# Optimization experiments

Measured on AMD Instinct MI355X. Metric: run time of the kernel, lower is better.

The kernel has to match this reference:

```python
import jax, jax.numpy as jnp
import numpy as np

EPS = 1e-5
H = 6  # num_heads

def batchnorm(x, g, b):
    # BatchNorm1d over node dim using batch statistics (biased var, eps=1e-5)
    mu = x.mean(0)
    var = jnp.mean((x - mu) ** 2, 0)
    return (x - mu) * jax.lax.rsqrt(var + EPS) * g + b

def setup_inputs() -> dict:
    key = jax.random.key(0)
    ks = jax.random.split(key, 16)
    N, E, D = 20000, 200000, 384
    DH = 2 * D  # mlp hidden = dim * mlp_ratio(2.0)
    s = 0.05
    lin = lambda k, i, o: jax.random.normal(k, (i, o), jnp.float32) * s
    inp = {}
    inp['x'] = jax.random.normal(ks[0], (N, D), jnp.float32)
    inp['edge_index'] = jax.random.randint(ks[1], (2, E), 0, N)
    inp['edge_attr'] = jax.random.normal(ks[2], (E, D), jnp.float32)
    # norm1
    inp['g1'] = jnp.ones((D,), jnp.float32); inp['b1'] = jnp.zeros((D,), jnp.float32)
    # TransformerConv-style attention (concat=True, beta=False, edge_dim=D)
    inp['Wq'] = lin(ks[3], D, D); inp['bq'] = jnp.zeros((D,), jnp.float32)
    inp['Wk'] = lin(ks[4], D, D); inp['bk'] = jnp.zeros((D,), jnp.float32)
    inp['Wv'] = lin(ks[5], D, D); inp['bv'] = jnp.zeros((D,), jnp.float32)
    inp['We'] = lin(ks[6], D, D)  # lin_edge, no bias
    inp['Wskip'] = lin(ks[7], D, D); inp['bskip'] = jnp.zeros((D,), jnp.float32)
    # norm2
    inp['g2'] = jnp.ones((D,), jnp.float32); inp['b2'] = jnp.zeros((D,), jnp.float32)
    # Mlp
    inp['W1'] = lin(ks[8], D, DH); inp['bm1'] = jnp.zeros((DH,), jnp.float32)
    inp['W2'] = lin(ks[9], DH, D); inp['bm2'] = jnp.zeros((D,), jnp.float32)
    return inp

def reference(x, edge_index, edge_attr, g1, b1, Wq, bq, Wk, bk, Wv, bv, We, Wskip, bskip, g2, b2, W1, bm1, W2, bm2):
    N, D = x.shape
    Dh = D // H
    scale = 1.0 / jnp.sqrt(jnp.float32(Dh))
    h = batchnorm(x, g1, b1)
    q = (h @ Wq + bq).reshape(N, H, Dh)
    k = (h @ Wk + bk).reshape(N, H, Dh)
    v = (h @ Wv + bv).reshape(N, H, Dh)
    e = (edge_attr @ We).reshape(-1, H, Dh)  # [E,H,Dh]
    src, dst = edge_index[0], edge_index[1]
    ke = k[src] + e  # edge attr added to key
    ve = v[src] + e  # and to value (PyG TransformerConv)
    logits = jnp.einsum('ehd,ehd->eh', q[dst], ke) * scale  # [E,H]
    # segment softmax over incoming edges of each dst node
    m = jax.ops.segment_max(logits, dst, num_segments=N)
    a = jnp.exp(logits - m[dst])
    ssum = jax.ops.segment_sum(a, dst, num_segments=N)
    denom = ssum[dst]
    a = a / jnp.where(denom == 0, 1.0, denom)
    agg = jax.ops.segment_sum(a[:, :, None] * ve, dst, num_segments=N).reshape(N, D)
    attn = agg + (h @ Wskip + bskip)  # root skip (lin_skip)
    x = x + attn  # residual 1 (drop_path/dropout disabled in eval)
    h2 = batchnorm(x, g2, b2)
    mlp = jax.nn.gelu(h2 @ W1 + bm1, approximate=False) @ W2 + bm2
    return x + mlp
```

## Files before the change

kernel.cpp:

```cpp
#include <hip/hip_runtime.h>
#include <hip/hip_bf16.h>

#define DD 384
#define NH 6
#define DHID 768

typedef __attribute__((ext_vector_type(8))) short bf16x8;
typedef __attribute__((ext_vector_type(4))) float f32x4;

__device__ __forceinline__ void gload_lds16(const void* gsrc, void* ldst) {
  __builtin_amdgcn_global_load_lds((const __attribute__((address_space(1))) void*)gsrc,
                                   (__attribute__((address_space(3))) void*)ldst,
                                   16, 0, 0);
}

__device__ __forceinline__ float b2f(unsigned short u) {
  union { unsigned int i; float f; } c;
  c.i = (unsigned int)u << 16;
  return c.f;
}

__device__ __forceinline__ short f2bf(float x) {
  union { __hip_bfloat16 h; short s; } u;
  u.h = __float2bfloat16(x);
  return u.s;
}

__global__ __launch_bounds__(384) void bn_stats_k(const float* __restrict__ x, float* __restrict__ sums,
                                                  float* __restrict__ sq, int N, int rpb) {
  int d = threadIdx.x;
  int r0 = blockIdx.x * rpb;
  int r1 = min(r0 + rpb, N);
  float s = 0.f, ss = 0.f;
  for (int r = r0; r < r1; ++r) {
    float v = x[(size_t)r * DD + d];
    s += v; ss += v * v;
  }
  atomicAdd(&sums[d], s);
  atomicAdd(&sq[d], ss);
}

__global__ void bn_finalize_k(const float* sums, const float* sq, const float* g, const float* b,
                              float* a, float* c, int N) {
  int d = blockIdx.x * blockDim.x + threadIdx.x;
  if (d >= DD) return;
  float inv = 1.f / (float)N;
  float mu = sums[d] * inv;
  float var = sq[d] * inv - mu * mu;
  float rs = rsqrtf(var + 1e-5f);
  a[d] = rs * g[d];
  c[d] = b[d] - mu * rs * g[d];
}

union BPack { ushort4 u; __hip_bfloat16 b[4]; };

__global__ void norm_to_bf16_k(const float* __restrict__ x, const float* __restrict__ a,
                               const float* __restrict__ c, __hip_bfloat16* __restrict__ h, int total4) {
  int i = blockIdx.x * blockDim.x + threadIdx.x;
  if (i >= total4) return;
  float4 v = ((const float4*)x)[i];
  int d0 = (i * 4) % DD;
  float4 av = *(const float4*)(a + d0);
  float4 cv = *(const float4*)(c + d0);
  BPack p;
  p.b[0] = __float2bfloat16(v.x * av.x + cv.x);
  p.b[1] = __float2bfloat16(v.y * av.y + cv.y);
  p.b[2] = __float2bfloat16(v.z * av.z + cv.z);
  p.b[3] = __float2bfloat16(v.w * av.w + cv.w);
  ((ushort4*)h)[i] = p.u;
}

__global__ void transpose_bf16_k(const float* __restrict__ in, __hip_bfloat16* __restrict__ out,
                                 int K, int Nout) {
  int i = blockIdx.x * blockDim.x + threadIdx.x;
  if (i >= K * Nout) return;
  int k = i / Nout, n = i % Nout;
  out[(size_t)n * K + k] = __float2bfloat16(in[i]);
}

__global__ void concat_bias_k(const float* bq, const float* bk, const float* bv, const float* bs,
                              float* out) {
  int i = blockIdx.x * blockDim.x + threadIdx.x;
  if (i >= 1536) return;
  float v = (i < 384) ? bq[i] : (i < 768) ? bk[i - 384] : (i < 1152) ? bv[i - 768] : bs[i - 1152];
  out[i] = v;
}

__global__ void add3_k(const float* __restrict__ x, const float* __restrict__ agg,
                       const float* __restrict__ skip, float* __restrict__ x1, int total4) {
  int i = blockIdx.x * blockDim.x + threadIdx.x;
  if (i >= total4) return;
  float4 a = ((const float4*)x)[i];
  float4 b = ((const float4*)agg)[i];
  float4 c = ((const float4*)skip)[i];
  float4 o;
  o.x = a.x + b.x + c.x; o.y = a.y + b.y + c.y;
  o.z = a.z + b.z + c.z; o.w = a.w + b.w + c.w;
  ((float4*)x1)[i] = o;
}

__global__ void hist_k(const int* __restrict__ ei, int* __restrict__ deg, int E) {
  int i = blockIdx.x * blockDim.x + threadIdx.x;
  if (i < E) atomicAdd(&deg[ei[E + i]], 1);
}

__global__ __launch_bounds__(1024) void scan_k(const int* __restrict__ deg, int* __restrict__ row_start,
                                               int* __restrict__ cursor, int N) {
  __shared__ int part[1024];
  int t = threadIdx.x;
  int ch = (N + 1023) / 1024;
  int c0 = t * ch, c1 = min(c0 + ch, N);
  int s = 0;
  for (int i = c0; i < c1; ++i) s += deg[i];
  part[t] = s;
  __syncthreads();
  for (int off = 1; off < 1024; off <<= 1) {
    int v = (t >= off) ? part[t - off] : 0;
    __syncthreads();
    part[t] += v;
    __syncthreads();
  }
  int run = part[t] - s;
  for (int i = c0; i < c1; ++i) {
    row_start[i] = run; cursor[i] = run; run += deg[i];
  }
  if (t == 1023) row_start[N] = part[1023];
}

__global__ void scatter_k(const int* __restrict__ ei, int* __restrict__ cursor,
                          int* __restrict__ csr_src, int* __restrict__ csr_eid, int E) {
  int i = blockIdx.x * blockDim.x + threadIdx.x;
  if (i >= E) return;
  int s = ei[i], d = ei[E + i];
  int pos = atomicAdd(&cursor[d], 1);
  csr_src[pos] = s;
  csr_eid[pos] = i;
}

__global__ __launch_bounds__(256) void attn_k(const __hip_bfloat16* __restrict__ qkv,
                                              const __hip_bfloat16* __restrict__ ebuf,
                                              const int* __restrict__ row_start,
                                              const int* __restrict__ csr_src,
                                              const int* __restrict__ csr_eid,
                                              float* __restrict__ agg, int N) {
  int wid = (blockIdx.x * blockDim.x + threadIdx.x) >> 6;
  int lane = threadIdx.x & 63;
  if (wid >= N) return;
  int g = lane >> 4, l = lane & 15;
  const ushort* qk = (const ushort*)qkv;
  const ushort* eu = (const ushort*)ebuf;
  float q[NH][4], acc[NH][4], psum[NH];
#pragma unroll
  for (int h = 0; h < NH; ++h) {
    ushort4 u = *(const ushort4*)&qk[(size_t)wid * 1152 + h * 64 + l * 4];
    q[h][0] = b2f(u.x); q[h][1] = b2f(u.y); q[h][2] = b2f(u.z); q[h][3] = b2f(u.w);
#pragma unroll
    for (int j = 0; j < 4; ++j) acc[h][j] = 0.f;
    psum[h] = 0.f;
  }
  int i0 = row_start[wid], i1 = row_start[wid + 1];
  for (int i = i0; i < i1; i += 4) {
    int e = i + g;
    bool valid = e < i1;
    int ec = valid ? e : i1 - 1;
    size_t sb = (size_t)csr_src[ec] * 1152;
    size_t eb = (size_t)csr_eid[ec] * 384;
    float ev[NH][4], p[NH];
#pragma unroll
    for (int h = 0; h < NH; ++h) {
      ushort4 ue = *(const ushort4*)&eu[eb + h * 64 + l * 4];
      ev[h][0] = b2f(ue.x); ev[h][1] = b2f(ue.y); ev[h][2] = b2f(ue.z); ev[h][3] = b2f(ue.w);
      ushort4 uk = *(const ushort4*)&qk[sb + 384 + h * 64 + l * 4];
      float t = q[h][0] * (b2f(uk.x) + ev[h][0]);
      t += q[h][1] * (b2f(uk.y) + ev[h][1]);
      t += q[h][2] * (b2f(uk.z) + ev[h][2]);
      t += q[h][3] * (b2f(uk.w) + ev[h][3]);
      t += __shfl_xor(t, 1);
      t += __shfl_xor(t, 2);
      t += __shfl_xor(t, 4);
      t += __shfl_xor(t, 8);
      p[h] = valid ? __expf(t * 0.125f) : 0.f;
    }
#pragma unroll
    for (int h = 0; h < NH; ++h) {
      ushort4 uv = *(const ushort4*)&qk[sb + 768 + h * 64 + l * 4];
      acc[h][0] += p[h] * (b2f(uv.x) + ev[h][0]);
      acc[h][1] += p[h] * (b2f(uv.y) + ev[h][1]);
      acc[h][2] += p[h] * (b2f(uv.z) + ev[h][2]);
      acc[h][3] += p[h] * (b2f(uv.w) + ev[h][3]);
      psum[h] += p[h];
    }
  }
#pragma unroll
  for (int h = 0; h < NH; ++h) {
#pragma unroll
    for (int j = 0; j < 4; ++j) {
      acc[h][j] += __shfl_xor(acc[h][j], 16);
      acc[h][j] += __shfl_xor(acc[h][j], 32);
    }
    psum[h] += __shfl_xor(psum[h], 16);
    psum[h] += __shfl_xor(psum[h], 32);
  }
  if (lane < 16) {
#pragma unroll
    for (int h = 0; h < NH; ++h) {
      float inv = psum[h] > 0.f ? 1.f / psum[h] : 0.f;
      float4 o;
      o.x = acc[h][0] * inv; o.y = acc[h][1] * inv;
      o.z = acc[h][2] * inv; o.w = acc[h][3] * inv;
      *(float4*)&agg[(size_t)wid * DD + h * 64 + l * 4] = o;
    }
  }
}

#define BM 128
#define BN 128
#define BK 64

enum { M_QKVS = 0, M_BF16 = 1, M_GELU = 2, M_RES = 3 };

template <int MODE>
__global__ __launch_bounds__(256) void gemm_k(const __hip_bfloat16* __restrict__ A,
                                              const __hip_bfloat16* __restrict__ BT,
                                              const float* __restrict__ bias,
                                              const float* __restrict__ res,
                                              void* __restrict__ out0, void* __restrict__ out1,
                                              int M, int K, int Nn) {
  __shared__ short lA[BM * BK];
  __shared__ short lB[BN * BK];
  int t = threadIdx.x;
  int lane = t & 63, w = t >> 6;
  int wr = (w >> 1) * 64, wc = (w & 1) * 64;
  int row0 = blockIdx.y * BM, col0 = blockIdx.x * BN;
  int lr = lane & 15, lk = lane >> 4;
  f32x4 acc[4][4] = {};

  for (int kt = 0; kt < K; kt += BK) {
    __syncthreads();
#pragma unroll
    for (int j = 0; j < 4; ++j) {
      int c = j * 256 + t;
      int r = c >> 3;
      int kcs = (c & 7) ^ (r & 7);
      int wavebase = (j * 256 + w * 64) * 8;
      int gra = row0 + r; gra = gra < M ? gra : M - 1;
      gload_lds16(A + (size_t)gra * K + kt + kcs * 8, &lA[wavebase]);
      gload_lds16(BT + (size_t)(col0 + r) * K + kt + kcs * 8, &lB[wavebase]);
    }
    __syncthreads();
#pragma unroll
    for (int kk = 0; kk < 2; ++kk) {
      int p = (kk * 4 + lk) ^ (lr & 7);
      bf16x8 af[4], bfr[4];
#pragma unroll
      for (int mi = 0; mi < 4; ++mi)
        af[mi] = *(const bf16x8*)&lA[(wr + mi * 16 + lr) * BK + p * 8];
#pragma unroll
      for (int ni = 0; ni < 4; ++ni)
        bfr[ni] = *(const bf16x8*)&lB[(wc + ni * 16 + lr) * BK + p * 8];
#pragma unroll
      for (int mi = 0; mi < 4; ++mi)
#pragma unroll
        for (int ni = 0; ni < 4; ++ni)
          acc[mi][ni] = __builtin_amdgcn_mfma_f32_16x16x32_bf16(af[mi], bfr[ni], acc[mi][ni], 0, 0, 0);
    }
  }

#pragma unroll
  for (int mi = 0; mi < 4; ++mi) {
#pragma unroll
    for (int r = 0; r < 4; ++r) {
      int row = row0 + wr + mi * 16 + lk * 4 + r;
      if (row >= M) continue;
#pragma unroll
      for (int ni = 0; ni < 4; ++ni) {
        int col = col0 + wc + ni * 16 + lr;
        float v = acc[mi][ni][r];
        if constexpr (MODE == M_QKVS) {
          v += bias[col];
          if (col < 1152)
            ((__hip_bfloat16*)out0)[(size_t)row * 1152 + col] = __float2bfloat16(v);
          else
            ((float*)out1)[(size_t)row * DD + (col - 1152)] = v;
        } else if constexpr (MODE == M_BF16) {
          ((__hip_bfloat16*)out0)[(size_t)row * Nn + col] = __float2bfloat16(v);
        } else if constexpr (MODE == M_GELU) {
          v += bias[col];
          v = 0.5f * v * (1.f + erff(v * 0.70710678118f));
          ((__hip_bfloat16*)out0)[(size_t)row * Nn + col] = __float2bfloat16(v);
        } else {
          v += bias[col];
          ((float*)out0)[(size_t)row * Nn + col] = v + res[(size_t)row * Nn + col];
        }
      }
    }
  }
}

__global__ __launch_bounds__(256, 2) void gemm_edge_wide(const float* __restrict__ A,
                                                         const __hip_bfloat16* __restrict__ BT,
                                                         __hip_bfloat16* __restrict__ out, int M) {
  __shared__ short lA[BM * BK];
  __shared__ short lB[DD * BK];
  int t = threadIdx.x;
  int lane = t & 63, w = t >> 6;
  int wr = (w >> 1) * 64, wc = (w & 1) * 192;
  int row0 = blockIdx.x * BM;
  int lr = lane & 15, lk = lane >> 4;
  f32x4 acc[4][12] = {};

  for (int kt = 0; kt < DD; kt += BK) {
    __syncthreads();
#pragma unroll
    for (int pss = 0; pss < 12; ++pss) {
      int c = pss * 256 + t;
      int r = c >> 3;
      int kcs = (c & 7) ^ (r & 7);
      int wavebase = (pss * 256 + w * 64) * 8;
      gload_lds16(BT + (size_t)r * DD + kt + kcs * 8, &lB[wavebase]);
    }
#pragma unroll
    for (int pss = 0; pss < 4; ++pss) {
      int c = pss * 256 + t;
      int r = c >> 3, kcl = c & 7;
      int gra = row0 + r; gra = gra < M ? gra : M - 1;
      const float4* ap = (const float4*)(A + (size_t)gra * DD + kt + kcl * 8);
      float4 f0 = ap[0], f1 = ap[1];
      bf16x8 v;
      v[0] = f2bf(f0.x); v[1] = f2bf(f0.y); v[2] = f2bf(f0.z); v[3] = f2bf(f0.w);
      v[4] = f2bf(f1.x); v[5] = f2bf(f1.y); v[6] = f2bf(f1.z); v[7] = f2bf(f1.w);
      *(__shared__ bf16x8*)&lA[r * BK + (kcl ^ (r & 7)) * 8] = v;
    }
    __syncthreads();
#pragma unroll
    for (int kk = 0; kk < 2; ++kk) {
      int p = (kk * 4 + lk) ^ (lr & 7);
      bf16x8 af[4];
#pragma unroll
      for (int mi = 0; mi < 4; ++mi)
        af[mi] = *(const bf16x8*)&lA[(wr + mi * 16 + lr) * BK + p * 8];
#pragma unroll
      for (int ni = 0; ni < 12; ++ni) {
        bf16x8 bfr = *(const bf16x8*)&lB[(wc + ni * 16 + lr) * BK + p * 8];
#pragma unroll
        for (int mi = 0; mi < 4; ++mi)
          acc[mi][ni] = __builtin_amdgcn_mfma_f32_16x16x32_bf16(af[mi], bfr, acc[mi][ni], 0, 0, 0);
      }
    }
  }

#pragma unroll
  for (int mi = 0; mi < 4; ++mi) {
#pragma unroll
    for (int r = 0; r < 4; ++r) {
      int row = row0 + wr + mi * 16 + lk * 4 + r;
      if (row >= M) continue;
#pragma unroll
      for (int ni = 0; ni < 12; ++ni) {
        int col = wc + ni * 16 + lr;
        out[(size_t)row * DD + col] = __float2bfloat16(acc[mi][ni][r]);
      }
    }
  }
}

extern "C" void kernel_launch(void* const* d_in, const int* in_sizes, int n_in,
                              void* d_out, int out_size, void* d_ws, size_t ws_size,
                              hipStream_t stream) {
  const float* x   = (const float*)d_in[0];
  const int*   ei  = (const int*)d_in[1];
  const float* ea  = (const float*)d_in[2];
  const float* g1  = (const float*)d_in[3];
  const float* b1  = (const float*)d_in[4];
  const float* Wq  = (const float*)d_in[5];
  const float* bq  = (const float*)d_in[6];
  const float* Wk  = (const float*)d_in[7];
  const float* bk  = (const float*)d_in[8];
  const float* Wv  = (const float*)d_in[9];
  const float* bv  = (const float*)d_in[10];
  const float* We  = (const float*)d_in[11];
  const float* Wsk = (const float*)d_in[12];
  const float* bsk = (const float*)d_in[13];
  const float* g2  = (const float*)d_in[14];
  const float* b2  = (const float*)d_in[15];
  const float* W1  = (const float*)d_in[16];
  const float* bm1 = (const float*)d_in[17];
  const float* W2  = (const float*)d_in[18];
  const float* bm2 = (const float*)d_in[19];

  int N = in_sizes[0] / DD;
  int E = in_sizes[1] / 2;

  char* ws = (char*)d_ws;
  size_t off = 0;
  auto alloc = [&](size_t bytes) -> char* {
    char* p = ws + off;
    off = (off + bytes + 255) & ~(size_t)255;
    return p;
  };

  float* bnsum = (float*)alloc(4 * DD * sizeof(float));
  float* a1 = (float*)alloc(DD * 4);
  float* c1 = (float*)alloc(DD * 4);
  float* a2 = (float*)alloc(DD * 4);
  float* c2 = (float*)alloc(DD * 4);
  float* bqkvs = (float*)alloc(1536 * 4);
  __hip_bfloat16* WqkvsT = (__hip_bfloat16*)alloc((size_t)1536 * DD * 2);
  __hip_bfloat16* WeT = (__hip_bfloat16*)alloc((size_t)DD * DD * 2);
  __hip_bfloat16* W1T = (__hip_bfloat16*)alloc((size_t)DHID * DD * 2);
  __hip_bfloat16* W2T = (__hip_bfloat16*)alloc((size_t)DD * DHID * 2);
  __hip_bfloat16* hbuf = (__hip_bfloat16*)alloc((size_t)N * DD * 2);
  __hip_bfloat16* qkv = (__hip_bfloat16*)alloc((size_t)N * 1152 * 2);
  float* skip = (float*)alloc((size_t)N * DD * 4);
  __hip_bfloat16* ebuf = (__hip_bfloat16*)alloc((size_t)E * DD * 2);
  float* agg = (float*)alloc((size_t)N * DD * 4);
  float* x1 = (float*)alloc((size_t)N * DD * 4);
  __hip_bfloat16* hid = (__hip_bfloat16*)alloc((size_t)N * DHID * 2);
  int* deg = (int*)alloc((size_t)N * 4);
  int* cursor = (int*)alloc((size_t)N * 4);
  int* row_start = (int*)alloc((size_t)(N + 1) * 4);
  int* csr_src = (int*)alloc((size_t)E * 4);
  int* csr_eid = (int*)alloc((size_t)E * 4);
  (void)ws_size; (void)n_in; (void)out_size;

  hipMemsetAsync(bnsum, 0, 4 * DD * sizeof(float), stream);
  hipMemsetAsync(deg, 0, (size_t)N * 4, stream);

  int rpb = 128, sgrid = (N + rpb - 1) / rpb;
  bn_stats_k<<<sgrid, DD, 0, stream>>>(x, bnsum, bnsum + DD, N, rpb);
  bn_finalize_k<<<2, 256, 0, stream>>>(bnsum, bnsum + DD, g1, b1, a1, c1, N);

  int t4 = N * DD / 4;
  norm_to_bf16_k<<<(t4 + 255) / 256, 256, 0, stream>>>(x, a1, c1, hbuf, t4);

  int wgrid = (DD * DD + 255) / 256;
  transpose_bf16_k<<<wgrid, 256, 0, stream>>>(Wq, WqkvsT, DD, DD);
  transpose_bf16_k<<<wgrid, 256, 0, stream>>>(Wk, WqkvsT + (size_t)DD * DD, DD, DD);
  transpose_bf16_k<<<wgrid, 256, 0, stream>>>(Wv, WqkvsT + (size_t)2 * DD * DD, DD, DD);
  transpose_bf16_k<<<wgrid, 256, 0, stream>>>(Wsk, WqkvsT + (size_t)3 * DD * DD, DD, DD);
  transpose_bf16_k<<<wgrid, 256, 0, stream>>>(We, WeT, DD, DD);
  transpose_bf16_k<<<(DD * DHID + 255) / 256, 256, 0, stream>>>(W1, W1T, DD, DHID);
  transpose_bf16_k<<<(DHID * DD + 255) / 256, 256, 0, stream>>>(W2, W2T, DHID, DD);
  concat_bias_k<<<6, 256, 0, stream>>>(bq, bk, bv, bsk, bqkvs);

  dim3 gqkvs(1536 / BN, (N + BM - 1) / BM);
  gemm_k<M_QKVS><<<gqkvs, 256, 0, stream>>>(hbuf, WqkvsT, bqkvs, nullptr, qkv, skip, N, DD, 1536);

  gemm_edge_wide<<<(E + BM - 1) / BM, 256, 0, stream>>>(ea, WeT, ebuf, E);

  hist_k<<<(E + 255) / 256, 256, 0, stream>>>(ei, deg, E);
  scan_k<<<1, 1024, 0, stream>>>(deg, row_start, cursor, N);
  scatter_k<<<(E + 255) / 256, 256, 0, stream>>>(ei, cursor, csr_src, csr_eid, E);

  attn_k<<<(N * 64 + 255) / 256, 256, 0, stream>>>(qkv, ebuf, row_start, csr_src, csr_eid, agg, N);

  add3_k<<<(t4 + 255) / 256, 256, 0, stream>>>(x, agg, skip, x1, t4);

  bn_stats_k<<<sgrid, DD, 0, stream>>>(x1, bnsum + 2 * DD, bnsum + 3 * DD, N, rpb);
  bn_finalize_k<<<2, 256, 0, stream>>>(bnsum + 2 * DD, bnsum + 3 * DD, g2, b2, a2, c2, N);
  norm_to_bf16_k<<<(t4 + 255) / 256, 256, 0, stream>>>(x1, a2, c2, hbuf, t4);

  dim3 gm1(DHID / BN, (N + BM - 1) / BM);
  gemm_k<M_GELU><<<gm1, 256, 0, stream>>>(hbuf, W1T, bm1, nullptr, hid, nullptr, N, DD, DHID);

  dim3 gm2(DD / BN, (N + BM - 1) / BM);
  gemm_k<M_RES><<<gm2, 256, 0, stream>>>(hid, W2T, bm2, x1, (float*)d_out, nullptr, N, DHID, DD);
}
```

Before: 605.5 us.

## Double-buffer LDS in GEMM kernels and load fp32 edge tiles directly to LDS

Both GEMM kernels now use two LDS buffers with BK halved to 32, prefetching the next K-tile with global_load_lds while MFMAs run on the current tile, and use one barrier per iteration. The edge GEMM also stops converting fp32 edge_attr to bf16 in registers before writing to LDS. It now DMA-loads the fp32 tile straight into a swizzled LDS buffer and converts to bf16 when building fragments. The aim is to hide global load latency and the register round-trip, at the cost of twice as many K iterations and barriers. The B tile also loses its XOR swizzle, which may cause LDS bank conflicts.

```diff
diff --git a/kernel.cpp b/kernel.cpp
--- a/kernel.cpp
+++ b/kernel.cpp
@@ -215,7 +215,7 @@
 
 #define BM 128
 #define BN 128
-#define BK 64
+#define BK 32
 
 enum { M_QKVS = 0, M_BF16 = 1, M_GELU = 2, M_RES = 3 };
 
@@ -226,8 +226,8 @@
                                               const float* __restrict__ res,
                                               void* __restrict__ out0, void* __restrict__ out1,
                                               int M, int K, int Nn) {
-  __shared__ short lA[BM * BK];
-  __shared__ short lB[BN * BK];
+  __shared__ short lA[2][BM * BK];
+  __shared__ short lB[2][BN * BK];
   int t = threadIdx.x;
   int lane = t & 63, w = t >> 6;
   int wr = (w >> 1) * 64, wc = (w & 1) * 64;
@@ -235,35 +235,39 @@
   int lr = lane & 15, lk = lane >> 4;
   f32x4 acc[4][4] = {};
 
-  for (int kt = 0; kt < K; kt += BK) {
-    __syncthreads();
-#pragma unroll
-    for (int j = 0; j < 4; ++j) {
-      int c = j * 256 + t;
-      int r = c >> 3;
-      int kcs = (c & 7) ^ (r & 7);
+  auto stage = [&](int b, int kt) {
+#pragma unroll
+    for (int j = 0; j < 2; ++j) {
+      int chunk = j * 256 + t;
+      int r = chunk >> 2, kc = chunk & 3;
       int wavebase = (j * 256 + w * 64) * 8;
       int gra = row0 + r; gra = gra < M ? gra : M - 1;
-      gload_lds16(A + (size_t)gra * K + kt + kcs * 8, &lA[wavebase]);
-      gload_lds16(BT + (size_t)(col0 + r) * K + kt + kcs * 8, &lB[wavebase]);
-    }
-    __syncthreads();
-#pragma unroll
-    for (int kk = 0; kk < 2; ++kk) {
-      int p = (kk * 4 + lk) ^ (lr & 7);
-      bf16x8 af[4], bfr[4];
-#pragma unroll
-      for (int mi = 0; mi < 4; ++mi)
-        af[mi] = *(const bf16x8*)&lA[(wr + mi * 16 + lr) * BK + p * 8];
+      gload_lds16(A + (size_t)gra * K + kt + kc * 8, &lA[b][wavebase]);
+      gload_lds16(BT + (size_t)(col0 + r) * K + kt + kc * 8, &lB[b][wavebase]);
+    }
+  };
+
+  stage(0, 0);
+  asm volatile("s_waitcnt vmcnt(0)" ::: "memory");
+  __builtin_amdgcn_s_barrier();
+  int nt = K / BK, cur = 0;
+  for (int ti = 0; ti < nt; ++ti) {
+    if (ti + 1 < nt) stage(cur ^ 1, (ti + 1) * BK);
+    bf16x8 af[4], bfr[4];
+#pragma unroll
+    for (int mi = 0; mi < 4; ++mi)
+      af[mi] = *(const bf16x8*)&lA[cur][(wr + mi * 16 + lr) * BK + lk * 8];
+#pragma unroll
+    for (int ni = 0; ni < 4; ++ni)
+      bfr[ni] = *(const bf16x8*)&lB[cur][(wc + ni * 16 + lr) * BK + lk * 8];
+#pragma unroll
+    for (int mi = 0; mi < 4; ++mi)
 #pragma unroll
       for (int ni = 0; ni < 4; ++ni)
-        bfr[ni] = *(const bf16x8*)&lB[(wc + ni * 16 + lr) * BK + p * 8];
-#pragma unroll
-      for (int mi = 0; mi < 4; ++mi)
-#pragma unroll
-        for (int ni = 0; ni < 4; ++ni)
-          acc[mi][ni] = __builtin_amdgcn_mfma_f32_16x16x32_bf16(af[mi], bfr[ni], acc[mi][ni], 0, 0, 0);
-    }
+        acc[mi][ni] = __builtin_amdgcn_mfma_f32_16x16x32_bf16(af[mi], bfr[ni], acc[mi][ni], 0, 0, 0);
+    asm volatile("s_waitcnt vmcnt(0)" ::: "memory");
+    __builtin_amdgcn_s_barrier();
+    cur ^= 1;
   }
 
 #pragma unroll
@@ -300,8 +304,8 @@
 __global__ __launch_bounds__(256, 2) void gemm_edge_wide(const float* __restrict__ A,
                                                          const __hip_bfloat16* __restrict__ BT,
                                                          __hip_bfloat16* __restrict__ out, int M) {
-  __shared__ short lA[BM * BK];
-  __shared__ short lB[DD * BK];
+  __shared__ float lAf[2][BM * BK];
+  __shared__ short lB[2][DD * BK];
   int t = threadIdx.x;
   int lane = t & 63, w = t >> 6;
   int wr = (w >> 1) * 64, wc = (w & 1) * 192;
@@ -309,44 +313,53 @@
   int lr = lane & 15, lk = lane >> 4;
   f32x4 acc[4][12] = {};
 
-  for (int kt = 0; kt < DD; kt += BK) {
-    __syncthreads();
-#pragma unroll
-    for (int pss = 0; pss < 12; ++pss) {
+  auto stage = [&](int b, int kt) {
+#pragma unroll
+    for (int pss = 0; pss < 6; ++pss) {
       int c = pss * 256 + t;
-      int r = c >> 3;
-      int kcs = (c & 7) ^ (r & 7);
+      int r = c >> 2, kc = c & 3;
       int wavebase = (pss * 256 + w * 64) * 8;
-      gload_lds16(BT + (size_t)r * DD + kt + kcs * 8, &lB[wavebase]);
+      gload_lds16(BT + (size_t)r * DD + kt + kc * 8, &lB[b][wavebase]);
     }
 #pragma unroll
     for (int pss = 0; pss < 4; ++pss) {
       int c = pss * 256 + t;
-      int r = c >> 3, kcl = c & 7;
+      int r = c >> 3, slot = c & 7;
+      int kc = slot ^ (r & 7);
       int gra = row0 + r; gra = gra < M ? gra : M - 1;
-      const float4* ap = (const float4*)(A + (size_t)gra * DD + kt + kcl * 8);
-      float4 f0 = ap[0], f1 = ap[1];
+      int wavebase = (pss * 256 + w * 64) * 4;
+      gload_lds16(A + (size_t)gra * DD + kt + kc * 4, &lAf[b][wavebase]);
+    }
+  };
+
+  stage(0, 0);
+  asm volatile("s_waitcnt vmcnt(0)" ::: "memory");
+  __builtin_amdgcn_s_barrier();
+  int nt = DD / BK, cur = 0;
+  for (int ti = 0; ti < nt; ++ti) {
+    if (ti + 1 < nt) stage(cur ^ 1, (ti + 1) * BK);
+    bf16x8 af[4];
+#pragma unroll
+    for (int mi = 0; mi < 4; ++mi) {
+      int r = wr + mi * 16 + lr;
+      int base = r * BK;
+      float4 fa = *(const float4*)&lAf[cur][base + (((2 * lk)) ^ (lr & 7)) * 4];
+      float4 fb = *(const float4*)&lAf[cur][base + (((2 * lk + 1)) ^ (lr & 7)) * 4];
       bf16x8 v;
-      v[0] = f2bf(f0.x); v[1] = f2bf(f0.y); v[2] = f2bf(f0.z); v[3] = f2bf(f0.w);
-      v[4] = f2bf(f1.x); v[5] = f2bf(f1.y); v[6] = f2bf(f1.z); v[7] = f2bf(f1.w);
-      *(__shared__ bf16x8*)&lA[r * BK + (kcl ^ (r & 7)) * 8] = v;
-    }
-    __syncthreads();
-#pragma unroll
-    for (int kk = 0; kk < 2; ++kk) {
-      int p = (kk * 4 + lk) ^ (lr & 7);
-      bf16x8 af[4];
+      v[0] = f2bf(fa.x); v[1] = f2bf(fa.y); v[2] = f2bf(fa.z); v[3] = f2bf(fa.w);
+      v[4] = f2bf(fb.x); v[5] = f2bf(fb.y); v[6] = f2bf(fb.z); v[7] = f2bf(fb.w);
+      af[mi] = v;
+    }
+#pragma unroll
+    for (int ni = 0; ni < 12; ++ni) {
+      bf16x8 bfr = *(const bf16x8*)&lB[cur][(wc + ni * 16 + lr) * BK + lk * 8];
 #pragma unroll
       for (int mi = 0; mi < 4; ++mi)
-        af[mi] = *(const bf16x8*)&lA[(wr + mi * 16 + lr) * BK + p * 8];
-#pragma unroll
-      for (int ni = 0; ni < 12; ++ni) {
-        bf16x8 bfr = *(const bf16x8*)&lB[(wc + ni * 16 + lr) * BK + p * 8];
-#pragma unroll
-        for (int mi = 0; mi < 4; ++mi)
-          acc[mi][ni] = __builtin_amdgcn_mfma_f32_16x16x32_bf16(af[mi], bfr, acc[mi][ni], 0, 0, 0);
-      }
-    }
+        acc[mi][ni] = __builtin_amdgcn_mfma_f32_16x16x32_bf16(af[mi], bfr, acc[mi][ni], 0, 0, 0);
+    }
+    asm volatile("s_waitcnt vmcnt(0)" ::: "memory");
+    __builtin_amdgcn_s_barrier();
+    cur ^= 1;
   }
 
 #pragma unroll
```

Result: no change. 597.6 us (-1.3%).
